# Kernel optimization log

Hardware: AMD Instinct MI355X
Metric: run time of the kernel (lower is better)

## Reference

```python
import math
import jax, jax.numpy as jnp
import numpy as np

B, N, D, H = 4, 2048, 512, 8
HD = D // H


def setup_inputs() -> dict:
    key = jax.random.key(0)
    ks = jax.random.split(key, 7)
    w_scale = 1.0 / math.sqrt(D)  # keep logits in a sane range (like default init)
    return {
        "q": jax.random.normal(ks[0], (B, N, D), dtype=jnp.float32),
        "mask": jax.random.randint(ks[1], (B, N), 0, 2) == 1,  # True = masked key
        "attn_bias": jax.random.normal(ks[2], (B, N, N), dtype=jnp.float32),
        "Wq": jax.random.normal(ks[3], (D, D), dtype=jnp.float32) * w_scale,
        "Wk": jax.random.normal(ks[4], (D, D), dtype=jnp.float32) * w_scale,
        "Wv": jax.random.normal(ks[5], (D, D), dtype=jnp.float32) * w_scale,
        "Wo": jax.random.normal(ks[6], (D, D), dtype=jnp.float32) * w_scale,
    }


def _heads(v):
    # [B, N, D] -> [H, B, N, HD]  (mirrors reshape + movedim(-2, 0))
    b, n, d = v.shape
    return v.reshape(b, n, H, HD).transpose(2, 0, 1, 3)


def reference(q, mask, attn_bias, Wq, Wk, Wv, Wo):
    # Linear projections (torch Linear: x @ W.T)
    qh = _heads(q @ Wq.T)
    kh = _heads(q @ Wk.T)   # self-attention: h defaults to q
    vh = _heads(q @ Wv.T)
    # scores: [H, B, Nq, Nk]
    scores = jnp.einsum("hbqd,hbkd->hbqk", qh, kh) / math.sqrt(HD)
    scores = scores + attn_bias[None]                     # broadcast over heads
    scores = jnp.where(mask[None, :, None, :], -jnp.inf, scores)
    attn = jax.nn.softmax(scores, axis=-1)
    out = jnp.einsum("hbqk,hbkd->hbqd", attn, vh)         # [H, B, Nq, HD]
    out = out.transpose(1, 2, 0, 3).reshape(q.shape[0], q.shape[1], D)
    return out @ Wo.T
```

## Files before the change

### kernel.cpp

```cpp
#include <hip/hip_runtime.h>
#include <stdint.h>


typedef __attribute__((ext_vector_type(8))) short short8;
typedef __attribute__((ext_vector_type(4))) short short4v;
typedef __attribute__((ext_vector_type(4))) float f32x4;

#define DEV static __device__ __forceinline__

constexpr int Bc = 4, Nc = 2048, Dc = 512, Hc = 8, HDc = 64;
constexpr int Mc = Bc * Nc;
constexpr int QKVNc = 3 * Dc;
constexpr float L2E = 1.44269504f;

DEV short bf16cast(float f) {
  return (short)__builtin_bit_cast(unsigned short, (__bf16)f);
}
DEV unsigned cvt_pk_bf16(float a, float b) {
  unsigned short lb = __builtin_bit_cast(unsigned short, (__bf16)a);
  unsigned short hb = __builtin_bit_cast(unsigned short, (__bf16)b);
  return (unsigned)lb | ((unsigned)hb << 16);
}
DEV unsigned pack_shorts(short a, short b) {
  return (unsigned)(unsigned short)a | ((unsigned)(unsigned short)b << 16);
}
DEV short8 cvt8(float4 a, float4 b) {
  union { short8 s; uint4 u; } r;
  r.u.x = cvt_pk_bf16(a.x, a.y); r.u.y = cvt_pk_bf16(a.z, a.w);
  r.u.z = cvt_pk_bf16(b.x, b.y); r.u.w = cvt_pk_bf16(b.z, b.w);
  return r.s;
}
DEV float fast_exp2(float x) {
#if __has_builtin(__builtin_amdgcn_exp2f)
  return __builtin_amdgcn_exp2f(x);
#else
  return exp2f(x);
#endif
}
DEV void permswap32(unsigned& a, unsigned& b) {
  asm volatile("v_permlane32_swap_b32 %0, %1" : "+v"(a), "+v"(b));
}
DEV void gl_lds16(const short* g, short* l) {
  __builtin_amdgcn_global_load_lds(
      (const __attribute__((address_space(1))) void*)g,
      (__attribute__((address_space(3))) void*)l, 16, 0, 0);
}

template<bool A_F32, int BN, bool OUT_F32>
__global__ __launch_bounds__(256, 2) void gemm_bt(const void* __restrict__ Av,
                                                  const float* __restrict__ B0,
                                                  const float* __restrict__ B1,
                                                  const float* __restrict__ B2,
                                                  void* __restrict__ Cv,
                                                  int M, int N,
                                                  int qcols, float cscale) {
  constexpr int K = 512;
  constexpr int BG = BN / 32;
  constexpr int MT = (BN == 128) ? 4 : 2;
  constexpr int NT = 4;
  __shared__ __align__(16) short At[128 * 72];
  __shared__ __align__(16) short Bt[BN * 72];
  const int tid = threadIdx.x, lane = tid & 63, wv = tid >> 6;
  const int quad = lane >> 4, l16 = lane & 15;
  const int mbase = blockIdx.y * 128, nbase = blockIdx.x * BN;
  const int wr = (BN == 128) ? (wv >> 1) * 64 : wv * 32;
  const int wc = (BN == 128) ? (wv & 1) * 64 : 0;
  const float* Bsel = nbase < 512 ? B0 : (nbase < 1024 ? B1 : B2);
  const int col0 = nbase & 511;
  const float scale = (nbase < qcols) ? cscale : 1.0f;
  f32x4 acc[MT][NT] = {};
  float4 apf[4][2]; short8 aph[4];
  float4 bpf[BG][2];
#pragma unroll
  for (int i = 0; i < 4; i++) {
    int flat = i * 256 + tid, row = flat >> 3, ch8 = (flat & 7) * 8;
    if (A_F32) {
      const float* Af = (const float*)Av;
      apf[i][0] = *(const float4*)&Af[(size_t)(mbase + row) * K + ch8];
      apf[i][1] = *(const float4*)&Af[(size_t)(mbase + row) * K + ch8 + 4];
    } else {
      aph[i] = *(const short8*)&((const short*)Av)[(size_t)(mbase + row) * K + ch8];
    }
  }
#pragma unroll
  for (int i = 0; i < BG; i++) {
    int flat = i * 256 + tid, row = flat >> 3, ch8 = (flat & 7) * 8;
    bpf[i][0] = *(const float4*)&Bsel[(size_t)(col0 + row) * K + ch8];
    bpf[i][1] = *(const float4*)&Bsel[(size_t)(col0 + row) * K + ch8 + 4];
  }
  for (int k0 = 0; k0 < K; k0 += 64) {
    __syncthreads();
#pragma unroll
    for (int i = 0; i < 4; i++) {
      int flat = i * 256 + tid, row = flat >> 3, ch8 = (flat & 7) * 8;
      *(short8*)&At[row * 72 + ch8] = A_F32 ? cvt8(apf[i][0], apf[i][1]) : aph[i];
    }
#pragma unroll
    for (int i = 0; i < BG; i++) {
      int flat = i * 256 + tid, row = flat >> 3, ch8 = (flat & 7) * 8;
      *(short8*)&Bt[row * 72 + ch8] = cvt8(bpf[i][0], bpf[i][1]);
    }
    if (k0 + 64 < K) {
#pragma unroll
      for (int i = 0; i < 4; i++) {
        int flat = i * 256 + tid, row = flat >> 3, ch8 = (flat & 7) * 8;
        if (A_F32) {
          const float* Af = (const float*)Av;
          apf[i][0] = *(const float4*)&Af[(size_t)(mbase + row) * K + k0 + 64 + ch8];
          apf[i][1] = *(const float4*)&Af[(size_t)(mbase + row) * K + k0 + 64 + ch8 + 4];
        } else {
          aph[i] = *(const short8*)&((const short*)Av)[(size_t)(mbase + row) * K + k0 + 64 + ch8];
        }
      }
#pragma unroll
      for (int i = 0; i < BG; i++) {
        int flat = i * 256 + tid, row = flat >> 3, ch8 = (flat & 7) * 8;
        bpf[i][0] = *(const float4*)&Bsel[(size_t)(col0 + row) * K + k0 + 64 + ch8];
        bpf[i][1] = *(const float4*)&Bsel[(size_t)(col0 + row) * K + k0 + 64 + ch8 + 4];
      }
    }
    __syncthreads();
#pragma unroll
    for (int s = 0; s < 2; s++) {
      short8 af[MT], bf[NT];
#pragma unroll
      for (int t = 0; t < MT; t++)
        af[t] = *(short8*)&At[(wr + t * 16 + l16) * 72 + quad * 8 + s * 32];
#pragma unroll
      for (int t = 0; t < NT; t++)
        bf[t] = *(short8*)&Bt[(wc + t * 16 + l16) * 72 + quad * 8 + s * 32];
#pragma unroll
      for (int mt = 0; mt < MT; mt++)
#pragma unroll
        for (int nt = 0; nt < NT; nt++)
          acc[mt][nt] = __builtin_amdgcn_mfma_f32_16x16x32_bf16(af[mt], bf[nt], acc[mt][nt], 0, 0, 0);
    }
  }
#pragma unroll
  for (int mt = 0; mt < MT; mt++)
#pragma unroll
    for (int nt = 0; nt < NT; nt++)
#pragma unroll
      for (int r = 0; r < 4; r++) {
        int row = mbase + wr + mt * 16 + quad * 4 + r;
        int col = nbase + wc + nt * 16 + l16;
        float v = acc[mt][nt][r] * scale;
        if (OUT_F32) ((float*)Cv)[(size_t)row * N + col] = v;
        else         ((short*)Cv)[(size_t)row * N + col] = bf16cast(v);
      }
}

__global__ __launch_bounds__(256, 2) void attn_kernel(const short* __restrict__ QKV,
                                                      const float* __restrict__ bias,
                                                      const void* __restrict__ mask,
                                                      short* __restrict__ Aout) {
  __shared__ __align__(16) short Kt[4][64 * 64];
  __shared__ __align__(16) short Vt[4][64 * 64];
  __shared__ __align__(16) float mlds[Nc];
  __shared__ int mflag;
  const int tid = threadIdx.x, lane = tid & 63, wv = tid >> 6;
  const int quad = lane >> 4, l16 = lane & 15;
  const int qt = blockIdx.x & 15, h = (blockIdx.x >> 4) & 7, b = (int)(blockIdx.x >> 7);
  const int qrow0 = qt * 128;
  const int q0 = qrow0 + wv * 32 + l16;
  const float* biasq0 = bias + ((size_t)b * Nc + q0) * Nc;
  const float* biasq1 = biasq0 + (size_t)16 * Nc;
  const short* Kbase = QKV + Dc + h * HDc;
  const short* Vbase = QKV + 2 * Dc + h * HDc;

#pragma unroll
  for (int j = 0; j < 2; j++)
#pragma unroll
    for (int g = 0; g < 2; g++) {
      int seg = wv * 2 + g, c = seg * 64 + lane;
      int row = c >> 3, ch = c & 7;
      gl_lds16(&Kbase[(size_t)(b * Nc + j * 64 + row) * QKVNc + ((ch ^ (row & 7)) << 3)],
               &Kt[j][seg * 512]);
    }

  short8 qf[2][2];
  {
    const short* qp0 = QKV + (size_t)(b * Nc + q0) * QKVNc + h * HDc + quad * 8;
    qf[0][0] = *(const short8*)qp0;
    qf[0][1] = *(const short8*)(qp0 + 32);
    const short* qp1 = qp0 + (size_t)16 * QKVNc;
    qf[1][0] = *(const short8*)qp1;
    qf[1][1] = *(const short8*)(qp1 + 32);
  }

  const int vp = tid & 31, vq = tid >> 5;
  const int vperm = (vp & 25) | ((vp & 4) >> 1) | ((vp & 2) << 1);
  const int vwbase = (((vperm >> 2)) << 3) + 2 * (vperm & 3);

  short8 v0pre[2], v1pre[2];
  float4 bpre[2][2][4];
#pragma unroll
  for (int j = 0; j < 2; j++) {
    v0pre[j] = *(const short8*)&Vbase[(size_t)(b * Nc + j * 64 + 2 * vp) * QKVNc + vq * 8];
    v1pre[j] = *(const short8*)&Vbase[(size_t)(b * Nc + j * 64 + 2 * vp + 1) * QKVNc + vq * 8];
#pragma unroll
    for (int t = 0; t < 4; t++) {
      bpre[j][0][t] = *(const float4*)&biasq0[j * 64 + t * 16 + quad * 4];
      bpre[j][1][t] = *(const float4*)&biasq1[j * 64 + t * 16 + quad * 4];
    }
  }

  if (tid == 0) mflag = 0;
  __syncthreads();
  {
    const uchar4* mw = (const uchar4*)((const char*)mask + (size_t)b * 2048);
    int acc = 0;
#pragma unroll
    for (int i = tid; i < 512; i += 256) {
      uchar4 v = mw[i];
      acc |= (int)v.y | (int)v.z | (int)v.w;
    }
    if (acc) atomicOr(&mflag, 1);
  }
  __syncthreads();
  {
    int isbyte = mflag;
    const unsigned char* mb = (const unsigned char*)mask + (size_t)b * 2048;
    const int* mi = (const int*)mask + (size_t)b * 2048;
    for (int i = tid; i < Nc; i += 256) {
      int v = isbyte ? (int)mb[i] : mi[i];
      mlds[i] = v ? -1e30f : 0.0f;
    }
  }

  const short ONEB = (short)0x3F80;
  const short8 ones = { ONEB, ONEB, ONEB, ONEB, ONEB, ONEB, ONEB, ONEB };

  f32x4 oacc[2][4] = {};
  f32x4 sumacc[2] = {};

  for (int pd = 0; pd < 16; pd++) {
    const int pb = (pd & 1) * 2;
    const int nb = 2 - pb;

#pragma unroll
    for (int j = 0; j < 2; j++)
#pragma unroll
      for (int jj = 0; jj < 8; jj++) {
        int hd = vq * 8 + jj;
        *(unsigned*)&Vt[pb + j][hd * 64 + (vwbase ^ ((hd & 7) << 3))] =
            pack_shorts(v0pre[j][jj], v1pre[j][jj]);
      }
    __syncthreads();

#pragma unroll
    for (int j = 0; j < 2; j++) {
      const int kn = ((2 * pd + 2 + j) & 31) * 64;
#pragma unroll
      for (int g = 0; g < 2; g++) {
        int seg = wv * 2 + g, c = seg * 64 + lane;
        int row = c >> 3, ch = c & 7;
        gl_lds16(&Kbase[(size_t)(b * Nc + kn + row) * QKVNc + ((ch ^ (row & 7)) << 3)],
                 &Kt[nb + j][seg * 512]);
      }
      v0pre[j] = *(const short8*)&Vbase[(size_t)(b * Nc + kn + 2 * vp) * QKVNc + vq * 8];
      v1pre[j] = *(const short8*)&Vbase[(size_t)(b * Nc + kn + 2 * vp + 1) * QKVNc + vq * 8];
    }

#pragma unroll
    for (int j = 0; j < 2; j++) {
      const int kb = (2 * pd + j) * 64;
      const int knb = ((2 * pd + j + 2) & 31) * 64;

      f32x4 sacc[2][4];
#pragma unroll
      for (int t = 0; t < 4; t++) {
        float4 mv = *(const float4*)&mlds[kb + t * 16 + quad * 4];
        sacc[0][t][0] = mv.x; sacc[0][t][1] = mv.y; sacc[0][t][2] = mv.z; sacc[0][t][3] = mv.w;
        sacc[1][t] = sacc[0][t];
      }

      __builtin_amdgcn_s_setprio(1);
#pragma unroll
      for (int s = 0; s < 2; s++)
#pragma unroll
        for (int t = 0; t < 4; t++) {
          short8 kf = *(short8*)&Kt[pb + j][(t * 16 + l16) * 64 + (((quad + 4 * s) ^ (l16 & 7)) << 3)];
          sacc[0][t] = __builtin_amdgcn_mfma_f32_16x16x32_bf16(kf, qf[0][s], sacc[0][t], 0, 0, 0);
          sacc[1][t] = __builtin_amdgcn_mfma_f32_16x16x32_bf16(kf, qf[1][s], sacc[1][t], 0, 0, 0);
        }
      __builtin_amdgcn_s_setprio(0);

      short8 pf[2][2];
#pragma unroll
      for (int n = 0; n < 2; n++) {
        unsigned pw[4][2];
#pragma unroll
        for (int t = 0; t < 4; t++) {
          float p0 = fast_exp2(__builtin_fmaf(bpre[j][n][t].x, L2E, sacc[n][t][0]));
          float p1 = fast_exp2(__builtin_fmaf(bpre[j][n][t].y, L2E, sacc[n][t][1]));
          float p2 = fast_exp2(__builtin_fmaf(bpre[j][n][t].z, L2E, sacc[n][t][2]));
          float p3 = fast_exp2(__builtin_fmaf(bpre[j][n][t].w, L2E, sacc[n][t][3]));
          pw[t][0] = cvt_pk_bf16(p0, p1);
          pw[t][1] = cvt_pk_bf16(p2, p3);
        }
        permswap32(pw[0][0], pw[1][0]); permswap32(pw[0][1], pw[1][1]);
        permswap32(pw[2][0], pw[3][0]); permswap32(pw[2][1], pw[3][1]);
        union { unsigned u[4]; short8 s; }
            a0{{pw[0][0], pw[0][1], pw[1][0], pw[1][1]}},
            a1{{pw[2][0], pw[2][1], pw[3][0], pw[3][1]}};
        pf[n][0] = a0.s; pf[n][1] = a1.s;
      }

#pragma unroll
      for (int t = 0; t < 4; t++) {
        bpre[j][0][t] = *(const float4*)&biasq0[knb + t * 16 + quad * 4];
        bpre[j][1][t] = *(const float4*)&biasq1[knb + t * 16 + quad * 4];
      }

      __builtin_amdgcn_s_setprio(1);
#pragma unroll
      for (int s = 0; s < 2; s++) {
        sumacc[0] = __builtin_amdgcn_mfma_f32_16x16x32_bf16(pf[0][s], ones, sumacc[0], 0, 0, 0);
        sumacc[1] = __builtin_amdgcn_mfma_f32_16x16x32_bf16(pf[1][s], ones, sumacc[1], 0, 0, 0);
#pragma unroll
        for (int t = 0; t < 4; t++) {
          short8 vf = *(short8*)&Vt[pb + j][(t * 16 + l16) * 64 + (((quad + 4 * s) ^ (l16 & 7)) << 3)];
          oacc[0][t] = __builtin_amdgcn_mfma_f32_16x16x32_bf16(pf[0][s], vf, oacc[0][t], 0, 0, 0);
          oacc[1][t] = __builtin_amdgcn_mfma_f32_16x16x32_bf16(pf[1][s], vf, oacc[1][t], 0, 0, 0);
        }
      }
      __builtin_amdgcn_s_setprio(0);
    }
  }

#pragma unroll
  for (int m = 0; m < 2; m++)
#pragma unroll
    for (int r = 0; r < 4; r++) {
      float inv = 1.0f / sumacc[m][r];
      int row = b * Nc + qrow0 + wv * 32 + m * 16 + quad * 4 + r;
#pragma unroll
      for (int t = 0; t < 4; t++)
        Aout[(size_t)row * Dc + h * HDc + t * 16 + l16] = bf16cast(oacc[m][t][r] * inv);
    }
}

extern "C" void kernel_launch(void* const* d_in, const int* in_sizes, int n_in,
                              void* d_out, int out_size, void* d_ws, size_t ws_size,
                              hipStream_t stream) {
  const float* q    = (const float*)d_in[0];
  const void*  mask = d_in[1];
  const float* bias = (const float*)d_in[2];
  const float* Wq   = (const float*)d_in[3];
  const float* Wk   = (const float*)d_in[4];
  const float* Wv   = (const float*)d_in[5];
  const float* Wo   = (const float*)d_in[6];
  float* out = (float*)d_out;

  char* ws = (char*)d_ws;
  short* QKV  = (short*)ws;  ws += (size_t)Mc * QKVNc * 2;
  short* aout = (short*)ws;  ws += (size_t)Mc * Dc * 2;

  gemm_bt<true, 128, false><<<dim3(QKVNc / 128, Mc / 128), dim3(256), 0, stream>>>(
      (const void*)q, Wq, Wk, Wv, (void*)QKV, Mc, QKVNc, Dc, 0.125f * L2E);
  attn_kernel<<<dim3(Bc * Hc * 16), dim3(256), 0, stream>>>(QKV, bias, mask, aout);
  gemm_bt<false, 64, true><<<dim3(Dc / 64, Mc / 128), dim3(256), 0, stream>>>(
      (const void*)aout, Wo, Wo, Wo, (void*)out, Mc, Dc, 0, 1.0f);
}
```

Baseline: 248.2 us.

## Pre-convert weights to bf16 and stream GEMM operands via direct global-to-LDS loads

Adds a small kernel that converts all four weight matrices to bf16 once per call. The two projection GEMMs then load bf16 operands straight into swizzled, double-buffered LDS with global_load_lds instead of converting fp32 through registers. The QKV GEMM tile widens to 192 columns, and the output GEMM drops a barrier. This cuts per-tile conversion work and register staging, at the cost of an extra launch, extra weight traffic and more LDS per block.

```diff
diff --git a/kernel.cpp b/kernel.cpp
--- a/kernel.cpp
+++ b/kernel.cpp
@@ -45,108 +45,179 @@
       (const __attribute__((address_space(1))) void*)g,
       (__attribute__((address_space(3))) void*)l, 16, 0, 0);
 }
-
-template<bool A_F32, int BN, bool OUT_F32>
-__global__ __launch_bounds__(256, 2) void gemm_bt(const void* __restrict__ Av,
-                                                  const float* __restrict__ B0,
-                                                  const float* __restrict__ B1,
-                                                  const float* __restrict__ B2,
-                                                  void* __restrict__ Cv,
-                                                  int M, int N,
-                                                  int qcols, float cscale) {
+DEV void barrier_lgkm_only() {
+  asm volatile("s_waitcnt lgkmcnt(0)" ::: "memory");
+  __builtin_amdgcn_s_barrier();
+  __builtin_amdgcn_sched_barrier(0);
+}
+
+__global__ void cvtw_kernel(const float* __restrict__ Wq, const float* __restrict__ Wk,
+                            const float* __restrict__ Wv, const float* __restrict__ Wo,
+                            short* __restrict__ Wqkv, short* __restrict__ Wob) {
+  int which = blockIdx.x >> 8;
+  int j = (blockIdx.x & 255) * 256 + threadIdx.x;
+  const float* src = which == 0 ? Wq : which == 1 ? Wk : which == 2 ? Wv : Wo;
+  short* dst = (which == 3) ? Wob : Wqkv + which * (Dc * Dc);
+  float4 v = ((const float4*)src)[j];
+  short4v o = { bf16cast(v.x), bf16cast(v.y), bf16cast(v.z), bf16cast(v.w) };
+  ((short4v*)dst)[j] = o;
+}
+
+__global__ __launch_bounds__(256, 2) void gemm_qkv(const float* __restrict__ q,
+                                                   const short* __restrict__ Wqkv,
+                                                   short* __restrict__ QKV,
+                                                   float cscale) {
   constexpr int K = 512;
-  constexpr int BG = BN / 32;
-  constexpr int MT = (BN == 128) ? 4 : 2;
-  constexpr int NT = 4;
   __shared__ __align__(16) short At[128 * 72];
-  __shared__ __align__(16) short Bt[BN * 72];
+  __shared__ __align__(16) short Bt[2][192 * 64];
   const int tid = threadIdx.x, lane = tid & 63, wv = tid >> 6;
   const int quad = lane >> 4, l16 = lane & 15;
-  const int mbase = blockIdx.y * 128, nbase = blockIdx.x * BN;
-  const int wr = (BN == 128) ? (wv >> 1) * 64 : wv * 32;
-  const int wc = (BN == 128) ? (wv & 1) * 64 : 0;
-  const float* Bsel = nbase < 512 ? B0 : (nbase < 1024 ? B1 : B2);
-  const int col0 = nbase & 511;
-  const float scale = (nbase < qcols) ? cscale : 1.0f;
-  f32x4 acc[MT][NT] = {};
-  float4 apf[4][2]; short8 aph[4];
-  float4 bpf[BG][2];
+  const int mbase = blockIdx.y * 128, nbase = blockIdx.x * 192;
+  const int wr = (wv >> 1) * 64, wc = (wv & 1) * 96;
+  f32x4 acc[4][6] = {};
+  float4 apf[4][2];
 #pragma unroll
   for (int i = 0; i < 4; i++) {
     int flat = i * 256 + tid, row = flat >> 3, ch8 = (flat & 7) * 8;
-    if (A_F32) {
-      const float* Af = (const float*)Av;
-      apf[i][0] = *(const float4*)&Af[(size_t)(mbase + row) * K + ch8];
-      apf[i][1] = *(const float4*)&Af[(size_t)(mbase + row) * K + ch8 + 4];
-    } else {
-      aph[i] = *(const short8*)&((const short*)Av)[(size_t)(mbase + row) * K + ch8];
-    }
-  }
-#pragma unroll
-  for (int i = 0; i < BG; i++) {
-    int flat = i * 256 + tid, row = flat >> 3, ch8 = (flat & 7) * 8;
-    bpf[i][0] = *(const float4*)&Bsel[(size_t)(col0 + row) * K + ch8];
-    bpf[i][1] = *(const float4*)&Bsel[(size_t)(col0 + row) * K + ch8 + 4];
+    apf[i][0] = *(const float4*)&q[(size_t)(mbase + row) * K + ch8];
+    apf[i][1] = *(const float4*)&q[(size_t)(mbase + row) * K + ch8 + 4];
+  }
+#pragma unroll
+  for (int i = 0; i < 6; i++) {
+    int ibase = (wv * 6 + i) * 64;
+    int row = (ibase + lane) >> 3, ch = lane & 7;
+    gl_lds16(&Wqkv[(size_t)(nbase + row) * K + ((ch ^ (row & 7)) << 3)],
+             &Bt[0][ibase << 3]);
   }
   for (int k0 = 0; k0 < K; k0 += 64) {
+    const int cur = (k0 >> 6) & 1;
     __syncthreads();
 #pragma unroll
     for (int i = 0; i < 4; i++) {
       int flat = i * 256 + tid, row = flat >> 3, ch8 = (flat & 7) * 8;
-      *(short8*)&At[row * 72 + ch8] = A_F32 ? cvt8(apf[i][0], apf[i][1]) : aph[i];
-    }
-#pragma unroll
-    for (int i = 0; i < BG; i++) {
-      int flat = i * 256 + tid, row = flat >> 3, ch8 = (flat & 7) * 8;
-      *(short8*)&Bt[row * 72 + ch8] = cvt8(bpf[i][0], bpf[i][1]);
+      *(short8*)&At[row * 72 + ch8] = cvt8(apf[i][0], apf[i][1]);
     }
     if (k0 + 64 < K) {
+#pragma unroll
+      for (int i = 0; i < 6; i++) {
+        int ibase = (wv * 6 + i) * 64;
+        int row = (ibase + lane) >> 3, ch = lane & 7;
+        gl_lds16(&Wqkv[(size_t)(nbase + row) * K + k0 + 64 + ((ch ^ (row & 7)) << 3)],
+                 &Bt[cur ^ 1][ibase << 3]);
+      }
 #pragma unroll
       for (int i = 0; i < 4; i++) {
         int flat = i * 256 + tid, row = flat >> 3, ch8 = (flat & 7) * 8;
-        if (A_F32) {
-          const float* Af = (const float*)Av;
-          apf[i][0] = *(const float4*)&Af[(size_t)(mbase + row) * K + k0 + 64 + ch8];
-          apf[i][1] = *(const float4*)&Af[(size_t)(mbase + row) * K + k0 + 64 + ch8 + 4];
-        } else {
-          aph[i] = *(const short8*)&((const short*)Av)[(size_t)(mbase + row) * K + k0 + 64 + ch8];
-        }
-      }
-#pragma unroll
-      for (int i = 0; i < BG; i++) {
-        int flat = i * 256 + tid, row = flat >> 3, ch8 = (flat & 7) * 8;
-        bpf[i][0] = *(const float4*)&Bsel[(size_t)(col0 + row) * K + k0 + 64 + ch8];
-        bpf[i][1] = *(const float4*)&Bsel[(size_t)(col0 + row) * K + k0 + 64 + ch8 + 4];
-      }
-    }
-    __syncthreads();
+        apf[i][0] = *(const float4*)&q[(size_t)(mbase + row) * K + k0 + 64 + ch8];
+        apf[i][1] = *(const float4*)&q[(size_t)(mbase + row) * K + k0 + 64 + ch8 + 4];
+      }
+    }
+    barrier_lgkm_only();
 #pragma unroll
     for (int s = 0; s < 2; s++) {
-      short8 af[MT], bf[NT];
-#pragma unroll
-      for (int t = 0; t < MT; t++)
+      short8 af[4], bf[6];
+#pragma unroll
+      for (int t = 0; t < 4; t++)
         af[t] = *(short8*)&At[(wr + t * 16 + l16) * 72 + quad * 8 + s * 32];
 #pragma unroll
-      for (int t = 0; t < NT; t++)
-        bf[t] = *(short8*)&Bt[(wc + t * 16 + l16) * 72 + quad * 8 + s * 32];
-#pragma unroll
-      for (int mt = 0; mt < MT; mt++)
-#pragma unroll
-        for (int nt = 0; nt < NT; nt++)
+      for (int t = 0; t < 6; t++) {
+        int r = wc + t * 16 + l16;
+        bf[t] = *(short8*)&Bt[cur][r * 64 + (((quad + 4 * s) ^ (r & 7)) << 3)];
+      }
+#pragma unroll
+      for (int mt = 0; mt < 4; mt++)
+#pragma unroll
+        for (int nt = 0; nt < 6; nt++)
           acc[mt][nt] = __builtin_amdgcn_mfma_f32_16x16x32_bf16(af[mt], bf[nt], acc[mt][nt], 0, 0, 0);
     }
   }
 #pragma unroll
-  for (int mt = 0; mt < MT; mt++)
-#pragma unroll
-    for (int nt = 0; nt < NT; nt++)
+  for (int nt = 0; nt < 6; nt++) {
+    const float sc = (nbase + wc + nt * 16 < 512) ? cscale : 1.0f;
+#pragma unroll
+    for (int mt = 0; mt < 4; mt++)
 #pragma unroll
       for (int r = 0; r < 4; r++) {
         int row = mbase + wr + mt * 16 + quad * 4 + r;
         int col = nbase + wc + nt * 16 + l16;
-        float v = acc[mt][nt][r] * scale;
-        if (OUT_F32) ((float*)Cv)[(size_t)row * N + col] = v;
-        else         ((short*)Cv)[(size_t)row * N + col] = bf16cast(v);
+        QKV[(size_t)row * QKVNc + col] = bf16cast(acc[mt][nt][r] * sc);
+      }
+  }
+}
+
+__global__ __launch_bounds__(256, 2) void gemm_out(const short* __restrict__ aout,
+                                                   const short* __restrict__ Wob,
+                                                   float* __restrict__ out) {
+  constexpr int K = 512;
+  __shared__ __align__(16) short At[2][128 * 64];
+  __shared__ __align__(16) short Bt[2][64 * 64];
+  const int tid = threadIdx.x, lane = tid & 63, wv = tid >> 6;
+  const int quad = lane >> 4, l16 = lane & 15;
+  const int mbase = blockIdx.y * 128, nbase = blockIdx.x * 64;
+  const int wr = wv * 32;
+  f32x4 acc[2][4] = {};
+#pragma unroll
+  for (int i = 0; i < 4; i++) {
+    int ibase = (wv * 4 + i) * 64;
+    int row = (ibase + lane) >> 3, ch = lane & 7;
+    gl_lds16(&aout[(size_t)(mbase + row) * K + ((ch ^ (row & 7)) << 3)],
+             &At[0][ibase << 3]);
+  }
+#pragma unroll
+  for (int i = 0; i < 2; i++) {
+    int ibase = (wv * 2 + i) * 64;
+    int row = (ibase + lane) >> 3, ch = lane & 7;
+    gl_lds16(&Wob[(size_t)(nbase + row) * K + ((ch ^ (row & 7)) << 3)],
+             &Bt[0][ibase << 3]);
+  }
+  for (int k0 = 0; k0 < K; k0 += 64) {
+    const int cur = (k0 >> 6) & 1;
+    __syncthreads();
+    if (k0 + 64 < K) {
+#pragma unroll
+      for (int i = 0; i < 4; i++) {
+        int ibase = (wv * 4 + i) * 64;
+        int row = (ibase + lane) >> 3, ch = lane & 7;
+        gl_lds16(&aout[(size_t)(mbase + row) * K + k0 + 64 + ((ch ^ (row & 7)) << 3)],
+                 &At[cur ^ 1][ibase << 3]);
+      }
+#pragma unroll
+      for (int i = 0; i < 2; i++) {
+        int ibase = (wv * 2 + i) * 64;
+        int row = (ibase + lane) >> 3, ch = lane & 7;
+        gl_lds16(&Wob[(size_t)(nbase + row) * K + k0 + 64 + ((ch ^ (row & 7)) << 3)],
+                 &Bt[cur ^ 1][ibase << 3]);
+      }
+    }
+#pragma unroll
+    for (int s = 0; s < 2; s++) {
+      short8 af[2], bf[4];
+#pragma unroll
+      for (int t = 0; t < 2; t++) {
+        int r = wr + t * 16 + l16;
+        af[t] = *(short8*)&At[cur][r * 64 + (((quad + 4 * s) ^ (r & 7)) << 3)];
+      }
+#pragma unroll
+      for (int t = 0; t < 4; t++) {
+        int r = t * 16 + l16;
+        bf[t] = *(short8*)&Bt[cur][r * 64 + (((quad + 4 * s) ^ (r & 7)) << 3)];
+      }
+#pragma unroll
+      for (int mt = 0; mt < 2; mt++)
+#pragma unroll
+        for (int nt = 0; nt < 4; nt++)
+          acc[mt][nt] = __builtin_amdgcn_mfma_f32_16x16x32_bf16(af[mt], bf[nt], acc[mt][nt], 0, 0, 0);
+    }
+  }
+#pragma unroll
+  for (int mt = 0; mt < 2; mt++)
+#pragma unroll
+    for (int nt = 0; nt < 4; nt++)
+#pragma unroll
+      for (int r = 0; r < 4; r++) {
+        int row = mbase + wr + mt * 16 + quad * 4 + r;
+        int col = nbase + nt * 16 + l16;
+        out[(size_t)row * Dc + col] = acc[mt][nt][r];
       }
 }
 
@@ -354,12 +425,15 @@
   float* out = (float*)d_out;
 
   char* ws = (char*)d_ws;
+  short* Wqkv = (short*)ws;  ws += (size_t)QKVNc * Dc * 2;
+  short* Wob  = (short*)ws;  ws += (size_t)Dc * Dc * 2;
   short* QKV  = (short*)ws;  ws += (size_t)Mc * QKVNc * 2;
   short* aout = (short*)ws;  ws += (size_t)Mc * Dc * 2;
 
-  gemm_bt<true, 128, false><<<dim3(QKVNc / 128, Mc / 128), dim3(256), 0, stream>>>(
-      (const void*)q, Wq, Wk, Wv, (void*)QKV, Mc, QKVNc, Dc, 0.125f * L2E);
+  cvtw_kernel<<<dim3(1024), dim3(256), 0, stream>>>(Wq, Wk, Wv, Wo, Wqkv, Wob);
+
+  gemm_qkv<<<dim3(QKVNc / 192, Mc / 128), dim3(256), 0, stream>>>(
+      q, Wqkv, QKV, 0.125f * L2E);
   attn_kernel<<<dim3(Bc * Hc * 16), dim3(256), 0, stream>>>(QKV, bias, mask, aout);
-  gemm_bt<false, 64, true><<<dim3(Dc / 64, Mc / 128), dim3(256), 0, stream>>>(
-      (const void*)aout, Wo, Wo, Wo, (void*)out, Mc, Dc, 0, 1.0f);
-}
+  gemm_out<<<dim3(Dc / 64, Mc / 128), dim3(256), 0, stream>>>(aout, Wob, out);
+}
```

Measured after the change: 244.4 us. No clear change (-1.5%).
